# Optimization experiments

Measured on AMD Instinct MI355X. Metric: run time of the kernel, lower is better.

The kernel has to match this reference:

```python
import jax, jax.numpy as jnp
import numpy as np

E = 1024   # embed_dim
H = 16     # num_heads
D = E // H # head_dim
T, N, M, B = 1024, 1024, 1023, 4  # tgt len, leaves, tree nodes, batch


def setup_inputs() -> dict:
    key0 = jax.random.key(0)
    ks = jax.random.split(key0, 8)
    s = 1.0 / np.sqrt(E).astype(np.float32)  # xavier-ish scale
    return {
        "query": jax.random.normal(ks[0], (T, B, E), jnp.float32),
        "key": jax.random.normal(ks[1], (N, B, E), jnp.float32),
        "node_key": jax.random.normal(ks[2], (M, B, E), jnp.float32),
        "in_proj_weight": jax.random.normal(ks[3], (3 * E, E), jnp.float32) * s,
        "in_proj_bias": jnp.zeros((3 * E,), jnp.float32),
        "out_w": jax.random.normal(ks[4], (E, E), jnp.float32) * s,
        "out_b": jnp.zeros((E,), jnp.float32),
        "dw_w": jax.random.normal(ks[5], (H, E), jnp.float32) * s,
        "dw_b": jnp.zeros((H,), jnp.float32),
        "key_padding_mask": jnp.zeros((B, N), bool),
        "node_padding_mask": jnp.zeros((B, M), bool),
    }


def reference(query, key, node_key, in_proj_weight, in_proj_bias,
              out_w, out_b, dw_w, dw_b, key_padding_mask, node_padding_mask):
    t, b, e = query.shape
    n, m = key.shape[0], node_key.shape[0]
    d = e // H
    scaling = d ** -0.5
    # fused in-proj slices (F.linear: y = x W^T + bias)
    Wq, Wk, Wv = in_proj_weight[:e], in_proj_weight[e:2 * e], in_proj_weight[2 * e:]
    bq, bk, bv = in_proj_bias[:e], in_proj_bias[e:2 * e], in_proj_bias[2 * e:]
    q = (query @ Wq.T + bq) * scaling
    k = key @ Wk.T + bk
    v = key @ Wv.T + bv
    nk = node_key @ Wk.T + bk          # node_kv_same: nodes share kv projection
    nv = node_key @ Wv.T + bv

    def heads(x, L):  # [L,B,E] -> [B,H,L,D]
        return x.reshape(L, b, H, d).transpose(1, 2, 0, 3)

    qh, kh, vh = heads(q, t), heads(k, n), heads(v, n)
    nkh, nvh = heads(nk, m), heads(nv, m)

    # per-head affinity weights for merged stack nodes (dwstack, sigmoid act)
    dw = jax.nn.sigmoid(node_key @ dw_w.T + dw_b)   # [M,B,H]
    nvh = nvh * dw.transpose(1, 2, 0)[..., None]    # weighted node values

    s_leaf = jnp.einsum('bhtd,bhnd->bhtn', qh, kh)
    s_node = jnp.einsum('bhtd,bhmd->bhtm', qh, nkh)
    neg = jnp.finfo(s_leaf.dtype).min
    s_leaf = jnp.where(key_padding_mask[:, None, None, :], neg, s_leaf)
    s_node = jnp.where(node_padding_mask[:, None, None, :], neg, s_node)

    attn = jax.nn.softmax(jnp.concatenate([s_leaf, s_node], axis=-1), axis=-1)
    vals = jnp.concatenate([vh, nvh], axis=2)       # [B,H,N+M,D]
    o = jnp.einsum('bhts,bhsd->bhtd', attn, vals)   # [B,H,T,D]
    o = o.transpose(2, 0, 1, 3).reshape(t, b, e)
    return o @ out_w.T + out_b
```

## Files before the change

kernel.cpp:

```cpp
#include <hip/hip_runtime.h>
#include <cstdint>
#include <cstddef>

using short8 = __attribute__((ext_vector_type(8))) short;
using f32x4  = __attribute__((ext_vector_type(4))) float;

constexpr int T_ = 1024;
constexpr int N_ = 1024;
constexpr int M_ = 1023;
constexpr int B_ = 4;
constexpr int E_ = 1024;
constexpr int H_ = 16;
constexpr int D_ = 64;

#define MFMA16(a, b, c) __builtin_amdgcn_mfma_f32_16x16x32_bf16((a), (b), (c), 0, 0, 0)

__device__ __forceinline__ unsigned short f2bf(float f) {
    unsigned int u = __float_as_uint(f);
    u += 0x7FFF + ((u >> 16) & 1);
    return (unsigned short)(u >> 16);
}
__device__ __forceinline__ float bf2f(unsigned short s) {
    return __uint_as_float(((unsigned int)s) << 16);
}

__device__ __forceinline__ unsigned int cvt_pk_bf16(float lo, float hi) {
    unsigned int r;
    asm("v_cvt_pk_bf16_f32 %0, %1, %2" : "=v"(r) : "v"(lo), "v"(hi));
    return r;
}

typedef __attribute__((address_space(1))) const unsigned char gc_byte;
typedef __attribute__((address_space(3))) unsigned char lds_byte;
__device__ __forceinline__ void gload16(const void* g, void* lds) {
    __builtin_amdgcn_global_load_lds((gc_byte*)(uintptr_t)g,
                                     (lds_byte*)(unsigned int)(uintptr_t)lds,
                                     16, 0, 0);
}

__device__ __forceinline__ void conv_body(const float* __restrict__ src,
                                          unsigned short* __restrict__ dst,
                                          int i, int n)
{
    if (i + 4 <= n) {
        const float4 v = *reinterpret_cast<const float4*>(src + i);
        ushort4 o;
        o.x = f2bf(v.x); o.y = f2bf(v.y); o.z = f2bf(v.z); o.w = f2bf(v.w);
        *reinterpret_cast<ushort4*>(dst + i) = o;
    } else {
        for (int k = 0; k < 4; ++k)
            dst[i + k] = (i + k < n) ? f2bf(src[i + k]) : (unsigned short)0;
    }
}

__global__ void conv_all(const float* __restrict__ query,
                         const float* __restrict__ key,
                         const float* __restrict__ node_key,
                         const float* __restrict__ ipw,
                         const float* __restrict__ out_w,
                         unsigned short* __restrict__ xq,
                         unsigned short* __restrict__ xk,
                         unsigned short* __restrict__ xn,
                         unsigned short* __restrict__ wbf,
                         unsigned short* __restrict__ wohi,
                         unsigned short* __restrict__ wolo)
{
    const int blk = blockIdx.x;
    const int tid = threadIdx.x;
    if (blk < 4096) {
        conv_body(query, xq, (blk * 256 + tid) * 4, 4194304);
    } else if (blk < 8192) {
        conv_body(key, xk, ((blk - 4096) * 256 + tid) * 4, 4194304);
    } else if (blk < 12288) {
        conv_body(node_key, xn, ((blk - 8192) * 256 + tid) * 4, 4190208);
    } else if (blk < 15360) {
        conv_body(ipw, wbf, ((blk - 12288) * 256 + tid) * 4, 3145728);
    } else {
        const int i = ((blk - 15360) * 256 + tid) * 4;
        const float4 v = *reinterpret_cast<const float4*>(out_w + i);
        float a[4] = {v.x, v.y, v.z, v.w};
        ushort4 hi, lo;
        unsigned short h[4], l[4];
        #pragma unroll
        for (int k = 0; k < 4; ++k) {
            h[k] = f2bf(a[k]);
            l[k] = f2bf(a[k] - bf2f(h[k]));
        }
        hi.x = h[0]; hi.y = h[1]; hi.z = h[2]; hi.w = h[3];
        lo.x = l[0]; lo.y = l[1]; lo.z = l[2]; lo.w = l[3];
        *reinterpret_cast<ushort4*>(wohi + i) = hi;
        *reinterpret_cast<ushort4*>(wolo + i) = lo;
    }
}

__global__ void dw_kernel(const float* __restrict__ node_key,
                          const float* __restrict__ dw_w,
                          const float* __restrict__ dw_b,
                          float* __restrict__ dwb)
{
    __shared__ float rowbuf[E_];
    const int r = blockIdx.x;
    const int tid = threadIdx.x;
    for (int idx = tid; idx < E_; idx += 256)
        rowbuf[idx] = node_key[(size_t)r * E_ + idx];
    __syncthreads();
    const int h = tid >> 4;
    const int lane = tid & 15;
    float acc = 0.f;
    const float* wrow = dw_w + (size_t)h * E_;
    for (int k = lane; k < E_; k += 16)
        acc = fmaf(rowbuf[k], wrow[k], acc);
    acc += __shfl_xor(acc, 8);
    acc += __shfl_xor(acc, 4);
    acc += __shfl_xor(acc, 2);
    acc += __shfl_xor(acc, 1);
    if (lane == 0) {
        float x = acc + dw_b[h];
        dwb[(size_t)r * H_ + h] = 1.f / (1.f + __expf(-x));
    }
}

__global__ __launch_bounds__(256) void proj_mfma(
    const unsigned short* __restrict__ xq,
    const unsigned short* __restrict__ xk,
    const unsigned short* __restrict__ xn,
    const unsigned short* __restrict__ wbf,
    const float* __restrict__ ipb,
    const float* __restrict__ dwb,
    unsigned short* __restrict__ qb,
    unsigned short* __restrict__ kb,
    unsigned short* __restrict__ vtb,
    unsigned short* __restrict__ nkb,
    unsigned short* __restrict__ nvtb)
{
    __shared__ unsigned short LDS[3][2][128 * 32];

    const unsigned short* A;
    const unsigned short* W;
    const float* bias;
    const float* dwm = nullptr;
    unsigned short* out;
    int epi;
    float scale = 1.f;
    switch (blockIdx.z) {
      case 0:  A = xq; W = wbf;           bias = ipb;        out = qb;   epi = 1; scale = 0.18033688011112042f; break;
      case 1:  A = xk; W = wbf + 1048576; bias = ipb + 1024; out = kb;   epi = 1; break;
      case 2:  A = xk; W = wbf + 2097152; bias = ipb + 2048; out = vtb;  epi = 2; break;
      case 3:  A = xn; W = wbf + 1048576; bias = ipb + 1024; out = nkb;  epi = 1; break;
      default: A = xn; W = wbf + 2097152; bias = ipb + 2048; out = nvtb; epi = 2; dwm = dwb; break;
    }

    const int tid = threadIdx.x;
    const int l = tid & 63, w = tid >> 6;
    const int brow = blockIdx.y * 128;
    const int bcol = blockIdx.x * 128;

    const int ch0 = w * 64 + l;
    const int ch1 = 256 + w * 64 + l;
    const int u0 = ((ch0 & 3) ^ ((ch0 >> 3) & 3)) * 8;
    const int u1 = ((ch1 & 3) ^ ((ch1 >> 3) & 3)) * 8;
    const unsigned short* gA0 = A + (size_t)(brow + (ch0 >> 2)) * E_ + u0;
    const unsigned short* gA1 = A + (size_t)(brow + (ch1 >> 2)) * E_ + u1;
    const unsigned short* gW0 = W + (size_t)(bcol + (ch0 >> 2)) * E_ + u0;
    const unsigned short* gW1 = W + (size_t)(bcol + (ch1 >> 2)) * E_ + u1;

    auto STAGE = [&](int buf, int kt) {
        gload16(gA0 + kt, &LDS[buf][0][(size_t)w * 512]);
        gload16(gA1 + kt, &LDS[buf][0][(size_t)(4 + w) * 512]);
        gload16(gW0 + kt, &LDS[buf][1][(size_t)w * 512]);
        gload16(gW1 + kt, &LDS[buf][1][(size_t)(4 + w) * 512]);
    };

    f32x4 acc[4][4];
    #pragma unroll
    for (int m = 0; m < 4; ++m)
        #pragma unroll
        for (int n = 0; n < 4; ++n)
            acc[m][n] = (f32x4){0.f, 0.f, 0.f, 0.f};

    const int wr = (w >> 1) * 64, wc = (w & 1) * 64;
    const int fr = l & 15;
    const int ko = (((l >> 4) ^ ((fr >> 1) & 3))) * 8;

    STAGE(0, 0);
    STAGE(1, 32);

    for (int t = 0; t < 32; ++t) {
        if (t < 31) asm volatile("s_waitcnt vmcnt(4)" ::: "memory");
        else        asm volatile("s_waitcnt vmcnt(0)" ::: "memory");
        __builtin_amdgcn_sched_barrier(0);
        __builtin_amdgcn_s_barrier();
        __builtin_amdgcn_sched_barrier(0);

        if (t < 30) STAGE((t + 2) % 3, (t + 2) * 32);

        const int cur = t % 3;
        short8 av[4], bv[4];
        #pragma unroll
        for (int m = 0; m < 4; ++m)
            av[m] = *reinterpret_cast<const short8*>(&LDS[cur][0][(wr + m * 16 + fr) * 32 + ko]);
        #pragma unroll
        for (int n = 0; n < 4; ++n)
            bv[n] = *reinterpret_cast<const short8*>(&LDS[cur][1][(wc + n * 16 + fr) * 32 + ko]);
        __builtin_amdgcn_s_setprio(1);
        #pragma unroll
        for (int m = 0; m < 4; ++m)
            #pragma unroll
            for (int n = 0; n < 4; ++n)
                acc[m][n] = MFMA16(av[m], bv[n], acc[m][n]);
        __builtin_amdgcn_s_setprio(0);
    }

    #pragma unroll
    for (int n = 0; n < 4; ++n) {
        const int c = bcol + wc + n * 16 + fr;
        const float bi = bias[c];
        #pragma unroll
        for (int m = 0; m < 4; ++m) {
            #pragma unroll
            for (int j = 0; j < 4; ++j) {
                const int r = brow + wr + m * 16 + (l >> 4) * 4 + j;
                float v = (acc[m][n][j] + bi) * scale;
                const int rn = r >> 2, b = r & 3, hh = c >> 6, dd = c & 63;
                if (epi == 1) {
                    out[((size_t)(b * H_ + hh) * 1024 + rn) * 64 + dd] = f2bf(v);
                } else {
                    if (dwm) v *= dwm[(size_t)r * H_ + hh];
                    out[(((size_t)(b * H_ + hh) * 32 + (rn >> 5)) * 64 + dd) * 32 + (rn & 31)] = f2bf(v);
                }
            }
        }
    }
}

__global__ __launch_bounds__(256) void outproj_mfma(
    const unsigned short* __restrict__ ahi,
    const unsigned short* __restrict__ whi,
    const unsigned short* __restrict__ wlo,
    const float* __restrict__ out_b,
    float* __restrict__ out)
{
    __shared__ unsigned short LDS[2][3][128 * 32];

    const int tid = threadIdx.x;
    const int l = tid & 63, w = tid >> 6;
    const int brow = blockIdx.y * 128;
    const int bcol = blockIdx.x * 128;

    const int ch0 = w * 64 + l;
    const int ch1 = 256 + w * 64 + l;
    const int u0 = ((ch0 & 3) ^ ((ch0 >> 3) & 3)) * 8;
    const int u1 = ((ch1 & 3) ^ ((ch1 >> 3) & 3)) * 8;
    const size_t ra0 = (size_t)(brow + (ch0 >> 2)) * E_ + u0;
    const size_t ra1 = (size_t)(brow + (ch1 >> 2)) * E_ + u1;
    const size_t rb0 = (size_t)(bcol + (ch0 >> 2)) * E_ + u0;
    const size_t rb1 = (size_t)(bcol + (ch1 >> 2)) * E_ + u1;

    auto STAGE = [&](int buf, int kt) {
        gload16(ahi + ra0 + kt, &LDS[buf][0][(size_t)w * 512]);
        gload16(ahi + ra1 + kt, &LDS[buf][0][(size_t)(4 + w) * 512]);
        gload16(whi + rb0 + kt, &LDS[buf][1][(size_t)w * 512]);
        gload16(whi + rb1 + kt, &LDS[buf][1][(size_t)(4 + w) * 512]);
        gload16(wlo + rb0 + kt, &LDS[buf][2][(size_t)w * 512]);
        gload16(wlo + rb1 + kt, &LDS[buf][2][(size_t)(4 + w) * 512]);
    };

    f32x4 acc[4][4];
    #pragma unroll
    for (int m = 0; m < 4; ++m)
        #pragma unroll
        for (int n = 0; n < 4; ++n)
            acc[m][n] = (f32x4){0.f, 0.f, 0.f, 0.f};

    const int wr = (w >> 1) * 64, wc = (w & 1) * 64;
    const int fr = l & 15;
    const int ko = (((l >> 4) ^ ((fr >> 1) & 3))) * 8;

    STAGE(0, 0);
    __syncthreads();
    for (int t = 0; t < 32; ++t) {
        const int cur = t & 1;
        if (t < 31) STAGE(cur ^ 1, (t + 1) * 32);
        short8 ah[4], bh[4], bl[4];
        #pragma unroll
        for (int m = 0; m < 4; ++m)
            ah[m] = *reinterpret_cast<const short8*>(&LDS[cur][0][(wr + m * 16 + fr) * 32 + ko]);
        #pragma unroll
        for (int n = 0; n < 4; ++n) {
            bh[n] = *reinterpret_cast<const short8*>(&LDS[cur][1][(wc + n * 16 + fr) * 32 + ko]);
            bl[n] = *reinterpret_cast<const short8*>(&LDS[cur][2][(wc + n * 16 + fr) * 32 + ko]);
        }
        __builtin_amdgcn_s_setprio(1);
        #pragma unroll
        for (int m = 0; m < 4; ++m)
            #pragma unroll
            for (int n = 0; n < 4; ++n) {
                acc[m][n] = MFMA16(ah[m], bh[n], acc[m][n]);
                acc[m][n] = MFMA16(ah[m], bl[n], acc[m][n]);
            }
        __builtin_amdgcn_s_setprio(0);
        if (t < 31) __syncthreads();
    }

    #pragma unroll
    for (int n = 0; n < 4; ++n) {
        const int c = bcol + wc + n * 16 + fr;
        const float bi = out_b[c];
        #pragma unroll
        for (int m = 0; m < 4; ++m)
            #pragma unroll
            for (int j = 0; j < 4; ++j) {
                const int r = brow + wr + m * 16 + (l >> 4) * 4 + j;
                out[(size_t)r * E_ + c] = acc[m][n][j] + bi;
            }
    }
}

__global__ __launch_bounds__(256) void attn_mfma(
    const unsigned short* __restrict__ qbf,
    const unsigned short* __restrict__ kbf,
    const unsigned short* __restrict__ nkbf,
    const unsigned short* __restrict__ vtb,
    const unsigned short* __restrict__ nvtb,
    const unsigned char* __restrict__ kpm,
    const unsigned char* __restrict__ npm,
    unsigned short* __restrict__ ohi)
{
    __shared__ unsigned short Kl[2][64 * 64];
    __shared__ unsigned short Vl[2][64 * 64];
    __shared__ unsigned short maskB[2048];
    __shared__ int tmask[32];

    const int tid = threadIdx.x;
    const int l = tid & 63, w = tid >> 6;
    const int bh = blockIdx.x, b = bh >> 4, h = bh & 15;
    const int t0 = blockIdx.y * 64;

    if (tid < 32) tmask[tid] = 0;
    __syncthreads();
    {
        const unsigned short negbf = f2bf(-60000.f);
        for (int s = tid; s < 2048; s += 256) {
            int masked;
            if (s < N_) masked = kpm[(size_t)b * N_ + s] ? 1 : 0;
            else {
                const int m = s - N_;
                masked = (m < M_ && !npm[(size_t)b * M_ + m]) ? 0 : 1;
            }
            maskB[s] = masked ? negbf : (unsigned short)0;
            if (masked) atomicOr(&tmask[s >> 6], 1);
        }
    }

    auto STAGE = [&](int buf, int s0) {
        const unsigned short* ksrc;
        const unsigned short* vsrc;
        int srow;
        if (s0 < N_) { ksrc = kbf;  vsrc = vtb;  srow = s0; }
        else         { ksrc = nkbf; vsrc = nvtb; srow = s0 - N_; }
        #pragma unroll
        for (int u = 0; u < 2; ++u) {
            const int c = u * 256 + tid;
            const int krow = c >> 3;
            const int kcol = ((c & 7) * 16) ^ ((krow & 7) << 4);
            gload16((const unsigned char*)ksrc +
                        ((size_t)(bh * 1024 + srow + krow) * 64) * 2 + kcol,
                    (unsigned char*)&Kl[buf][0] + c * 16);
            const int kg = c >> 6;
            const int dd = c & 63;
            const int kv = srow + kg * 8;
            const int kp = kv >> 5;
            gload16((const unsigned char*)vsrc +
                        (((size_t)(bh * 32 + kp) * 64 + dd) * 32 + (kv & 31)) * 2,
                    (unsigned char*)&Vl[buf][0] + c * 16);
        }
    };

    const int g = l >> 4;
    const int q = l & 15;

    const int qrow = t0 + w * 16 + q;
    const short8 aq0 = *reinterpret_cast<const short8*>(&qbf[((size_t)bh * T_ + qrow) * 64 + g * 8]);
    const short8 aq1 = *reinterpret_cast<const short8*>(&qbf[((size_t)bh * T_ + qrow) * 64 + 32 + g * 8]);

    float mold = -30000.f, lrp = 0.f;
    f32x4 acco[4];
    #pragma unroll
    for (int n = 0; n < 4; ++n) acco[n] = (f32x4){0.f, 0.f, 0.f, 0.f};

    const int ksw = (l & 7) << 4;
    const int kb0 = q * 128 + ((g * 16) ^ ksw);
    const int kb1 = q * 128 + ((64 + g * 16) ^ ksw);
    const int vb0 = g * 1024 + q * 16;

    const int src0 = (g & 1) * 32 + q;
    const int src1 = src0 + 16;
    const bool selhi = (l & 32) != 0;

    STAGE(0, 0);
    __syncthreads();

    for (int it = 0; it < 32; ++it) {
        const int s0 = it * 64;
        const int cur = it & 1;
        if (it < 31) STAGE(cur ^ 1, s0 + 64);

        const unsigned char* const Kc = (const unsigned char*)&Kl[cur][0];
        const unsigned char* const Vc = (const unsigned char*)&Vl[cur][0];

        f32x4 accs[4];
        #pragma unroll
        for (int n = 0; n < 4; ++n) accs[n] = (f32x4){0.f, 0.f, 0.f, 0.f};
        __builtin_amdgcn_s_setprio(1);
        #pragma unroll
        for (int n = 0; n < 4; ++n) {
            const short8 k0 = *reinterpret_cast<const short8*>(Kc + n * 2048 + kb0);
            const short8 k1 = *reinterpret_cast<const short8*>(Kc + n * 2048 + kb1);
            accs[n] = MFMA16(k0, aq0, accs[n]);
            accs[n] = MFMA16(k1, aq1, accs[n]);
        }
        __builtin_amdgcn_s_setprio(0);

        if (tmask[s0 >> 6]) {
            #pragma unroll
            for (int n = 0; n < 4; ++n) {
                const ushort4 mz = *reinterpret_cast<const ushort4*>(&maskB[s0 + n * 16 + g * 4]);
                accs[n][0] += bf2f(mz.x);
                accs[n][1] += bf2f(mz.y);
                accs[n][2] += bf2f(mz.z);
                accs[n][3] += bf2f(mz.w);
            }
        }

        float mx;
        {
            const float t0_ = fmaxf(fmaxf(accs[0][0], accs[0][1]), accs[0][2]);
            const float t1_ = fmaxf(fmaxf(accs[0][3], accs[1][0]), accs[1][1]);
            const float t2_ = fmaxf(fmaxf(accs[1][2], accs[1][3]), accs[2][0]);
            const float t3_ = fmaxf(fmaxf(accs[2][1], accs[2][2]), accs[2][3]);
            const float t4_ = fmaxf(fmaxf(accs[3][0], accs[3][1]), accs[3][2]);
            const float t5_ = fmaxf(fmaxf(t0_, t1_), t2_);
            const float t6_ = fmaxf(fmaxf(t3_, t4_), accs[3][3]);
            mx = fmaxf(t5_, t6_);
        }
        mx = fmaxf(mx, __shfl_xor(mx, 16));
        mx = fmaxf(mx, __shfl_xor(mx, 32));

        if (__any(mx > mold + 8.f)) {
            const float mn = fmaxf(mold, mx);
            const float f = __builtin_amdgcn_exp2f(mold - mn);
            mold = mn;
            lrp *= f;
            #pragma unroll
            for (int n = 0; n < 4; ++n)
                #pragma unroll
                for (int j = 0; j < 4; ++j) acco[n][j] *= f;
        }

        float p[4][4];
        float ps = 0.f;
        #pragma unroll
        for (int n = 0; n < 4; ++n)
            #pragma unroll
            for (int j = 0; j < 4; ++j) {
                p[n][j] = __builtin_amdgcn_exp2f(accs[n][j] - mold);
                ps += p[n][j];
            }
        lrp += ps;

        unsigned int ppk[4][2];
        #pragma unroll
        for (int n = 0; n < 4; ++n) {
            ppk[n][0] = cvt_pk_bf16(p[n][0], p[n][1]);
            ppk[n][1] = cvt_pk_bf16(p[n][2], p[n][3]);
        }

        union UF { int4 i4; short8 s8; } pf[2];
        #pragma unroll
        for (int hh2 = 0; hh2 < 2; ++hh2) {
            const unsigned int a0 = __shfl((int)ppk[2 * hh2][0],     src0);
            const unsigned int b0 = __shfl((int)ppk[2 * hh2 + 1][0], src0);
            const unsigned int a1 = __shfl((int)ppk[2 * hh2][1],     src0);
            const unsigned int b1 = __shfl((int)ppk[2 * hh2 + 1][1], src0);
            const unsigned int a2 = __shfl((int)ppk[2 * hh2][0],     src1);
            const unsigned int b2 = __shfl((int)ppk[2 * hh2 + 1][0], src1);
            const unsigned int a3 = __shfl((int)ppk[2 * hh2][1],     src1);
            const unsigned int b3 = __shfl((int)ppk[2 * hh2 + 1][1], src1);
            pf[hh2].i4.x = selhi ? b0 : a0;
            pf[hh2].i4.y = selhi ? b1 : a1;
            pf[hh2].i4.z = selhi ? b2 : a2;
            pf[hh2].i4.w = selhi ? b3 : a3;
        }

        __builtin_amdgcn_s_setprio(1);
        #pragma unroll
        for (int n = 0; n < 4; ++n) {
            const short8 v0 = *reinterpret_cast<const short8*>(Vc + n * 256 + vb0);
            const short8 v1 = *reinterpret_cast<const short8*>(Vc + 4096 + n * 256 + vb0);
            acco[n] = MFMA16(v0, pf[0].s8, acco[n]);
            acco[n] = MFMA16(v1, pf[1].s8, acco[n]);
        }
        __builtin_amdgcn_s_setprio(0);

        __syncthreads();
    }

    float lr = lrp;
    lr += __shfl_xor(lr, 16);
    lr += __shfl_xor(lr, 32);
    const float linv = 1.f / lr;
    const int t = t0 + w * 16 + q;
    const size_t obase = ((size_t)t * B_ + b) * E_ + h * 64;
    #pragma unroll
    for (int n = 0; n < 4; ++n) {
        ushort4 h4;
        h4.x = f2bf(acco[n][0] * linv);
        h4.y = f2bf(acco[n][1] * linv);
        h4.z = f2bf(acco[n][2] * linv);
        h4.w = f2bf(acco[n][3] * linv);
        *reinterpret_cast<ushort4*>(&ohi[obase + n * 16 + g * 4]) = h4;
    }
}

extern "C" void kernel_launch(void* const* d_in, const int* in_sizes, int n_in,
                              void* d_out, int out_size, void* d_ws, size_t ws_size,
                              hipStream_t stream) {
    const float* query    = (const float*)d_in[0];
    const float* key      = (const float*)d_in[1];
    const float* node_key = (const float*)d_in[2];
    const float* ipw      = (const float*)d_in[3];
    const float* ipb      = (const float*)d_in[4];
    const float* out_w    = (const float*)d_in[5];
    const float* out_b    = (const float*)d_in[6];
    const float* dw_w     = (const float*)d_in[7];
    const float* dw_b     = (const float*)d_in[8];
    const unsigned char* kpm = (const unsigned char*)d_in[9];
    const unsigned char* npm = (const unsigned char*)d_in[10];
    float* out = (float*)d_out;

    char* p = (char*)d_ws;
    auto alloc = [&](size_t bytes) {
        char* r = p;
        p += (bytes + 255) & ~(size_t)255;
        return r;
    };
    unsigned short* xq    = (unsigned short*)alloc((size_t)4096 * 1024 * 2);
    unsigned short* xk    = (unsigned short*)alloc((size_t)4096 * 1024 * 2);
    unsigned short* xn    = (unsigned short*)alloc((size_t)4096 * 1024 * 2);
    unsigned short* wbf   = (unsigned short*)alloc((size_t)3072 * 1024 * 2);
    unsigned short* wohi  = (unsigned short*)alloc((size_t)1024 * 1024 * 2);
    unsigned short* wolo  = (unsigned short*)alloc((size_t)1024 * 1024 * 2);
    unsigned short* qb    = (unsigned short*)alloc((size_t)64 * 1024 * 64 * 2);
    unsigned short* kb_   = (unsigned short*)alloc((size_t)64 * 1024 * 64 * 2);
    unsigned short* nkb   = (unsigned short*)alloc((size_t)64 * 1024 * 64 * 2);
    unsigned short* vtb   = (unsigned short*)alloc((size_t)64 * 1024 * 64 * 2);
    unsigned short* nvtb  = (unsigned short*)alloc((size_t)64 * 1024 * 64 * 2);
    unsigned short* ohi   = (unsigned short*)alloc((size_t)4096 * 1024 * 2);
    float*          dwb   = (float*)alloc((size_t)4096 * 16 * 4);

    const dim3 blk(256);

    conv_all<<<dim3(16384), blk, 0, stream>>>(query, key, node_key, ipw, out_w,
                                              xq, xk, xn, wbf, wohi, wolo);

    dw_kernel<<<dim3(M_ * B_), blk, 0, stream>>>(node_key, dw_w, dw_b, dwb);

    proj_mfma<<<dim3(8, 32, 5), blk, 0, stream>>>(xq, xk, xn, wbf, ipb, dwb,
                                                  qb, kb_, vtb, nkb, nvtb);

    attn_mfma<<<dim3(64, 16), blk, 0, stream>>>(qb, kb_, nkb, vtb, nvtb,
                                                kpm, npm, ohi);

    outproj_mfma<<<dim3(8, 32), blk, 0, stream>>>(ohi, wohi, wolo, out_b, out);
}
```

Measured before the change: 231.1 us.

## Load projection A fragments directly from global and fold dw kernel into conversion

The projection GEMM now loads the activation (A) operand fragments straight from global memory into registers, double-buffered across k-steps, and only stages the weight tile through LDS. This halves LDS traffic and footprint and removes the A-side LDS reads. The sigmoid affinity-weight computation is merged into the conversion kernel as extra blocks, which saves one kernel launch. In exchange, each wave's A reads from global are uncoalesced 16-byte row fragments duplicated across the two column-waves, the vmcnt accounting is more fragile, and the LDS rowbuf is now allocated for every conv block.

```diff
diff --git a/kernel.cpp b/kernel.cpp
--- a/kernel.cpp
+++ b/kernel.cpp
@@ -58,13 +58,17 @@
                          const float* __restrict__ node_key,
                          const float* __restrict__ ipw,
                          const float* __restrict__ out_w,
+                         const float* __restrict__ dw_w,
+                         const float* __restrict__ dw_b,
                          unsigned short* __restrict__ xq,
                          unsigned short* __restrict__ xk,
                          unsigned short* __restrict__ xn,
                          unsigned short* __restrict__ wbf,
                          unsigned short* __restrict__ wohi,
-                         unsigned short* __restrict__ wolo)
+                         unsigned short* __restrict__ wolo,
+                         float* __restrict__ dwb)
 {
+    __shared__ float rowbuf[E_];
     const int blk = blockIdx.x;
     const int tid = threadIdx.x;
     if (blk < 4096) {
@@ -75,7 +79,7 @@
         conv_body(node_key, xn, ((blk - 8192) * 256 + tid) * 4, 4190208);
     } else if (blk < 15360) {
         conv_body(ipw, wbf, ((blk - 12288) * 256 + tid) * 4, 3145728);
-    } else {
+    } else if (blk < 16384) {
         const int i = ((blk - 15360) * 256 + tid) * 4;
         const float4 v = *reinterpret_cast<const float4*>(out_w + i);
         float a[4] = {v.x, v.y, v.z, v.w};
@@ -90,33 +94,25 @@
         lo.x = l[0]; lo.y = l[1]; lo.z = l[2]; lo.w = l[3];
         *reinterpret_cast<ushort4*>(wohi + i) = hi;
         *reinterpret_cast<ushort4*>(wolo + i) = lo;
-    }
-}
-
-__global__ void dw_kernel(const float* __restrict__ node_key,
-                          const float* __restrict__ dw_w,
-                          const float* __restrict__ dw_b,
-                          float* __restrict__ dwb)
-{
-    __shared__ float rowbuf[E_];
-    const int r = blockIdx.x;
-    const int tid = threadIdx.x;
-    for (int idx = tid; idx < E_; idx += 256)
-        rowbuf[idx] = node_key[(size_t)r * E_ + idx];
-    __syncthreads();
-    const int h = tid >> 4;
-    const int lane = tid & 15;
-    float acc = 0.f;
-    const float* wrow = dw_w + (size_t)h * E_;
-    for (int k = lane; k < E_; k += 16)
-        acc = fmaf(rowbuf[k], wrow[k], acc);
-    acc += __shfl_xor(acc, 8);
-    acc += __shfl_xor(acc, 4);
-    acc += __shfl_xor(acc, 2);
-    acc += __shfl_xor(acc, 1);
-    if (lane == 0) {
-        float x = acc + dw_b[h];
-        dwb[(size_t)r * H_ + h] = 1.f / (1.f + __expf(-x));
+    } else {
+        const int r = blk - 16384;
+        for (int idx = tid; idx < E_; idx += 256)
+            rowbuf[idx] = node_key[(size_t)r * E_ + idx];
+        __syncthreads();
+        const int h = tid >> 4;
+        const int lane = tid & 15;
+        float acc = 0.f;
+        const float* wrow = dw_w + (size_t)h * E_;
+        for (int k = lane; k < E_; k += 16)
+            acc = fmaf(rowbuf[k], wrow[k], acc);
+        acc += __shfl_xor(acc, 8);
+        acc += __shfl_xor(acc, 4);
+        acc += __shfl_xor(acc, 2);
+        acc += __shfl_xor(acc, 1);
+        if (lane == 0) {
+            float x = acc + dw_b[h];
+            dwb[(size_t)r * H_ + h] = 1.f / (1.f + __expf(-x));
+        }
     }
 }
 
@@ -133,7 +129,7 @@
     unsigned short* __restrict__ nkb,
     unsigned short* __restrict__ nvtb)
 {
-    __shared__ unsigned short LDS[3][2][128 * 32];
+    __shared__ unsigned short LDS[3][4096];
 
     const unsigned short* A;
     const unsigned short* W;
@@ -159,16 +155,12 @@
     const int ch1 = 256 + w * 64 + l;
     const int u0 = ((ch0 & 3) ^ ((ch0 >> 3) & 3)) * 8;
     const int u1 = ((ch1 & 3) ^ ((ch1 >> 3) & 3)) * 8;
-    const unsigned short* gA0 = A + (size_t)(brow + (ch0 >> 2)) * E_ + u0;
-    const unsigned short* gA1 = A + (size_t)(brow + (ch1 >> 2)) * E_ + u1;
     const unsigned short* gW0 = W + (size_t)(bcol + (ch0 >> 2)) * E_ + u0;
     const unsigned short* gW1 = W + (size_t)(bcol + (ch1 >> 2)) * E_ + u1;
 
     auto STAGE = [&](int buf, int kt) {
-        gload16(gA0 + kt, &LDS[buf][0][(size_t)w * 512]);
-        gload16(gA1 + kt, &LDS[buf][0][(size_t)(4 + w) * 512]);
-        gload16(gW0 + kt, &LDS[buf][1][(size_t)w * 512]);
-        gload16(gW1 + kt, &LDS[buf][1][(size_t)(4 + w) * 512]);
+        gload16(gW0 + kt, &LDS[buf][(size_t)w * 512]);
+        gload16(gW1 + kt, &LDS[buf][(size_t)(4 + w) * 512]);
     };
 
     f32x4 acc[4][4];
@@ -182,34 +174,55 @@
     const int fr = l & 15;
     const int ko = (((l >> 4) ^ ((fr >> 1) & 3))) * 8;
 
+    const unsigned short* gA = A + (size_t)(brow + wr + fr) * E_ + (l >> 4) * 8;
+
+    short8 avA[4], avB[4];
+
+    #pragma unroll
+    for (int m = 0; m < 4; ++m)
+        avA[m] = *reinterpret_cast<const short8*>(gA + (size_t)m * 16 * E_);
     STAGE(0, 0);
     STAGE(1, 32);
-
-    for (int t = 0; t < 32; ++t) {
-        if (t < 31) asm volatile("s_waitcnt vmcnt(4)" ::: "memory");
-        else        asm volatile("s_waitcnt vmcnt(0)" ::: "memory");
-        __builtin_amdgcn_sched_barrier(0);
-        __builtin_amdgcn_s_barrier();
-        __builtin_amdgcn_sched_barrier(0);
-
-        if (t < 30) STAGE((t + 2) % 3, (t + 2) * 32);
-
-        const int cur = t % 3;
-        short8 av[4], bv[4];
-        #pragma unroll
-        for (int m = 0; m < 4; ++m)
-            av[m] = *reinterpret_cast<const short8*>(&LDS[cur][0][(wr + m * 16 + fr) * 32 + ko]);
-        #pragma unroll
-        for (int n = 0; n < 4; ++n)
-            bv[n] = *reinterpret_cast<const short8*>(&LDS[cur][1][(wc + n * 16 + fr) * 32 + ko]);
-        __builtin_amdgcn_s_setprio(1);
-        #pragma unroll
-        for (int m = 0; m < 4; ++m)
-            #pragma unroll
-            for (int n = 0; n < 4; ++n)
-                acc[m][n] = MFMA16(av[m], bv[n], acc[m][n]);
-        __builtin_amdgcn_s_setprio(0);
-    }
+    asm volatile("s_waitcnt vmcnt(2)" ::: "memory");
+
+#define PROJ_STEP(T, CUR, NXT)                                                  \
+    {                                                                           \
+        const int t_ = (T);                                                     \
+        if (t_ > 0) {                                                           \
+            if (t_ < 31) asm volatile("s_waitcnt vmcnt(2)" ::: "memory");       \
+            else         asm volatile("s_waitcnt vmcnt(0)" ::: "memory");       \
+        }                                                                       \
+        __builtin_amdgcn_sched_barrier(0);                                      \
+        __builtin_amdgcn_s_barrier();                                           \
+        __builtin_amdgcn_sched_barrier(0);                                      \
+        if (t_ < 31) {                                                          \
+            _Pragma("unroll")                                                   \
+            for (int m = 0; m < 4; ++m)                                         \
+                NXT[m] = *reinterpret_cast<const short8*>(                      \
+                    gA + (size_t)m * 16 * E_ + (t_ + 1) * 32);                  \
+        }                                                                       \
+        if (t_ < 30) STAGE((t_ + 2) % 3, (t_ + 2) * 32);                        \
+        __builtin_amdgcn_sched_barrier(0);                                      \
+        const int cur_ = t_ % 3;                                                \
+        short8 bv[4];                                                           \
+        _Pragma("unroll")                                                       \
+        for (int n = 0; n < 4; ++n)                                             \
+            bv[n] = *reinterpret_cast<const short8*>(                           \
+                &LDS[cur_][(wc + n * 16 + fr) * 32 + ko]);                      \
+        __builtin_amdgcn_s_setprio(1);                                          \
+        _Pragma("unroll")                                                       \
+        for (int m = 0; m < 4; ++m)                                             \
+            _Pragma("unroll")                                                   \
+            for (int n = 0; n < 4; ++n)                                         \
+                acc[m][n] = MFMA16(CUR[m], bv[n], acc[m][n]);                   \
+        __builtin_amdgcn_s_setprio(0);                                          \
+    }
+
+    for (int tt = 0; tt < 32; tt += 2) {
+        PROJ_STEP(tt,     avA, avB);
+        PROJ_STEP(tt + 1, avB, avA);
+    }
+#undef PROJ_STEP
 
     #pragma unroll
     for (int n = 0; n < 4; ++n) {
@@ -560,10 +573,9 @@
 
     const dim3 blk(256);
 
-    conv_all<<<dim3(16384), blk, 0, stream>>>(query, key, node_key, ipw, out_w,
-                                              xq, xk, xn, wbf, wohi, wolo);
-
-    dw_kernel<<<dim3(M_ * B_), blk, 0, stream>>>(node_key, dw_w, dw_b, dwb);
+    conv_all<<<dim3(16384 + 4092), blk, 0, stream>>>(
+        query, key, node_key, ipw, out_w, dw_w, dw_b,
+        xq, xk, xn, wbf, wohi, wolo, dwb);
 
     proj_mfma<<<dim3(8, 32, 5), blk, 0, stream>>>(xq, xk, xn, wbf, ipb, dwb,
                                                   qb, kb_, vtb, nkb, nvtb);
```

New measurement: 261.0 us. 12.9% more time.
